# Kernel tuning notes

Measured on AMD Instinct MI355X. Metric: run time of the kernel, lower is better.

## Reference

```python
import jax, jax.numpy as jnp
import numpy as np

N = 100000   # nodes
E = 1600000  # edges
F_IN = 4
H = 64
G = 1000     # graphs in batch
C = 3        # num_classes
L = 2        # num_unit (LEConv layers)


def setup_inputs() -> dict:
    key = jax.random.key(0)
    ks = jax.random.split(key, 14)
    s = 0.1
    return {
        "x": jax.random.normal(ks[0], (N, F_IN), jnp.float32),
        "edge_index": jax.random.randint(ks[1], (2, E), 0, N, dtype=jnp.int32),
        "edge_attr": jax.random.uniform(ks[2], (E,), jnp.float32),
        "batch": jnp.sort(jax.random.randint(ks[3], (N,), 0, G, dtype=jnp.int32)),
        "w_emb": jax.random.normal(ks[4], (F_IN, H), jnp.float32) * s,
        "b_emb": jnp.zeros((H,), jnp.float32),
        "lin1_w": jax.random.normal(ks[5], (L, H, H), jnp.float32) * s,
        "lin1_b": jnp.zeros((L, H), jnp.float32),
        "lin2_w": jax.random.normal(ks[6], (L, H, H), jnp.float32) * s,  # bias=False in PyG LEConv
        "lin3_w": jax.random.normal(ks[7], (L, H, H), jnp.float32) * s,
        "lin3_b": jnp.zeros((L, H), jnp.float32),
        "mlp_w1": jax.random.normal(ks[8], (H, 2 * H), jnp.float32) * s,
        "mlp_b1": jnp.zeros((2 * H,), jnp.float32),
        "mlp_w2": jax.random.normal(ks[9], (2 * H, C), jnp.float32) * s,
        "mlp_b2": jnp.zeros((C,), jnp.float32),
    }


def reference(x, edge_index, edge_attr, batch, w_emb, b_emb,
              lin1_w, lin1_b, lin2_w, lin3_w, lin3_b,
              mlp_w1, mlp_b1, mlp_w2, mlp_b2):
    src, dst = edge_index[0], edge_index[1]  # message flows src(j) -> dst(i)
    h = x @ w_emb + b_emb  # [N, H]
    for l in range(L):
        a = h @ lin1_w[l] + lin1_b[l]            # lin1(x_j) source side
        b = h @ lin2_w[l]                         # lin2(x_i) target side, no bias
        msg = (a[src] - b[dst]) * edge_attr[:, None]   # [E, H]
        agg = jax.ops.segment_sum(msg, dst, num_segments=N)
        h = jax.nn.relu(agg + h @ lin3_w[l] + lin3_b[l])
    # global_mean_pool
    sums = jax.ops.segment_sum(h, batch, num_segments=G)        # [G, H]
    counts = jax.ops.segment_sum(jnp.ones((N,), h.dtype), batch, num_segments=G)
    graph_x = sums / jnp.maximum(counts, 1.0)[:, None]
    # causal_mlp head
    return jax.nn.relu(graph_x @ mlp_w1 + mlp_b1) @ mlp_w2 + mlp_b2  # [G, C]
```

## Files before the change

### kernel.cpp

```cpp
#include <hip/hip_runtime.h>

#define N_NODES 100000
#define N_EDGES 1600000
#define F_INPUT 4
#define HDIM 64
#define G_GRAPHS 1000
#define C_CLS 3

#define NPB 256
#define BSHIFT 8
#define NB 391
#define CBLK 98
#define CSR_CAP 6144
#define EMB_BLOCKS 6250
#define HIST_BLOCKS 512
#define BNDS_BLOCKS 391

typedef __attribute__((ext_vector_type(8))) short bf16x8;
typedef __attribute__((ext_vector_type(4))) float f32x4;

__device__ __forceinline__ unsigned short f2bf(float f) {
    unsigned u = __float_as_uint(f);
    unsigned r = (u + 0x7FFF + ((u >> 16) & 1)) >> 16;
    return (unsigned short)r;
}
__device__ __forceinline__ float bflo(unsigned u) {
    return __uint_as_float(u << 16);
}
__device__ __forceinline__ float bfhi(unsigned u) {
    return __uint_as_float(u & 0xFFFF0000u);
}
__device__ __forceinline__ float bf1(unsigned short s) {
    return __uint_as_float(((unsigned)s) << 16);
}

__global__ __launch_bounds__(256) void k_emb_hist(
    const float* __restrict__ x, const float* __restrict__ w, const float* __restrict__ b,
    unsigned short* __restrict__ h, const int* __restrict__ dst, int* __restrict__ bcnt,
    const int* __restrict__ batch, int* __restrict__ goff) {
    __shared__ int s[NB];
    if (blockIdx.x < EMB_BLOCKS) {
        int t = blockIdx.x * 256 + threadIdx.x;
        int n = t >> 4, f0 = (t & 15) * 4;
        const float* xr = x + n * F_INPUT;
        float x0 = xr[0], x1 = xr[1], x2 = xr[2], x3 = xr[3];
        ushort4 o;
        {
            float a0 = b[f0+0] + x0*w[0*HDIM+f0+0] + x1*w[1*HDIM+f0+0] + x2*w[2*HDIM+f0+0] + x3*w[3*HDIM+f0+0];
            float a1 = b[f0+1] + x0*w[0*HDIM+f0+1] + x1*w[1*HDIM+f0+1] + x2*w[2*HDIM+f0+1] + x3*w[3*HDIM+f0+1];
            float a2 = b[f0+2] + x0*w[0*HDIM+f0+2] + x1*w[1*HDIM+f0+2] + x2*w[2*HDIM+f0+2] + x3*w[3*HDIM+f0+2];
            float a3 = b[f0+3] + x0*w[0*HDIM+f0+3] + x1*w[1*HDIM+f0+3] + x2*w[2*HDIM+f0+3] + x3*w[3*HDIM+f0+3];
            o.x = f2bf(a0); o.y = f2bf(a1); o.z = f2bf(a2); o.w = f2bf(a3);
        }
        *(ushort4*)(h + (size_t)n * HDIM + f0) = o;
    } else if (blockIdx.x < EMB_BLOCKS + HIST_BLOCKS) {
        int bb = blockIdx.x - EMB_BLOCKS;
        for (int i = threadIdx.x; i < NB; i += 256) s[i] = 0;
        __syncthreads();
        for (int e = bb * 256 + threadIdx.x; e < N_EDGES; e += HIST_BLOCKS * 256)
            atomicAdd(&s[dst[e] >> BSHIFT], 1);
        __syncthreads();
        for (int i = threadIdx.x; i < NB; i += 256)
            if (s[i]) atomicAdd(&bcnt[i], s[i]);
    } else {
        int n = (blockIdx.x - EMB_BLOCKS - HIST_BLOCKS) * 256 + threadIdx.x;
        if (n >= N_NODES) return;
        int bv = batch[n];
        int bp = (n == 0) ? -1 : batch[n - 1];
        for (int g = bp + 1; g <= bv; ++g) goff[g] = n;
        if (n == N_NODES - 1) {
            for (int g = bv + 1; g <= G_GRAPHS; ++g) goff[g] = N_NODES;
        }
    }
}

__global__ __launch_bounds__(512) void k_boff(
    const int* __restrict__ bcnt, int* __restrict__ boff, int* __restrict__ bcur) {
    __shared__ int s[512];
    int t = threadIdx.x;
    int v = (t < NB) ? bcnt[t] : 0;
    s[t] = v;
    __syncthreads();
    for (int d = 1; d < 512; d <<= 1) {
        int x2 = (t >= d) ? s[t - d] : 0;
        __syncthreads();
        s[t] += x2;
        __syncthreads();
    }
    int ex = s[t] - v;
    if (t < NB) { boff[t] = ex; bcur[t] = ex; }
    if (t == 0) boff[NB] = N_EDGES;
}

__global__ __launch_bounds__(1024) void k_bucket(const int* __restrict__ src,
                                                 const int* __restrict__ dst,
                                                 const float* __restrict__ attr,
                                                 int* __restrict__ bcur,
                                                 int2* __restrict__ bbuf) {
    __shared__ int cnt[NB];
    __shared__ int base[NB];
    for (int i = threadIdx.x; i < NB; i += 1024) cnt[i] = 0;
    __syncthreads();
    int e0 = blockIdx.x * 16384;
    int myb[16], myrank[16];
    int2 mypack[16];
#pragma unroll
    for (int k = 0; k < 16; ++k) {
        int e = e0 + k * 1024 + threadIdx.x;
        if (e < N_EDGES) {
            int d = dst[e];
            int b = d >> BSHIFT;
            myb[k] = b;
            myrank[k] = atomicAdd(&cnt[b], 1);
            mypack[k].x = src[e] | ((d & (NPB - 1)) << 17);
            mypack[k].y = __float_as_int(attr[e]);
        } else
            myb[k] = -1;
    }
    __syncthreads();
    for (int i = threadIdx.x; i < NB; i += 1024)
        base[i] = cnt[i] ? atomicAdd(&bcur[i], cnt[i]) : 0;
    __syncthreads();
#pragma unroll
    for (int k = 0; k < 16; ++k)
        if (myb[k] >= 0) bbuf[base[myb[k]] + myrank[k]] = mypack[k];
}

__global__ __launch_bounds__(256) void k_csr(const int2* __restrict__ bbuf,
                                             const int* __restrict__ boff,
                                             int* __restrict__ off,
                                             float* __restrict__ wsum,
                                             int2* __restrict__ edge2) {
    __shared__ int2 se[CSR_CAP];
    __shared__ int deg[NPB];
    __shared__ float wsm[NPB];
    __shared__ int loff[NPB];
    __shared__ int sct[256];
    int b = blockIdx.x;
    int lo = boff[b];
    int cnt = boff[b + 1] - lo;
    if (cnt > CSR_CAP) cnt = CSR_CAP;
    int t = threadIdx.x;
    deg[t] = 0;
    wsm[t] = 0.f;
    for (int i = t; i < cnt; i += 256) se[i] = bbuf[lo + i];
    __syncthreads();
    for (int i = t; i < cnt; i += 256) {
        int2 p = se[i];
        int dloc = (p.x >> 17) & (NPB - 1);
        atomicAdd(&deg[dloc], 1);
        atomicAdd(&wsm[dloc], __int_as_float(p.y));
    }
    __syncthreads();
    int v = deg[t];
    sct[t] = v;
    __syncthreads();
    for (int d = 1; d < 256; d <<= 1) {
        int x2 = (t >= d) ? sct[t - d] : 0;
        __syncthreads();
        sct[t] += x2;
        __syncthreads();
    }
    int ex = sct[t] - v;
    loff[t] = ex;
    __syncthreads();
    int n = b * NPB + t;
    if (n < N_NODES) { off[n] = lo + ex; wsum[n] = wsm[t]; }
    if (b == NB - 1 && t == 0) off[N_NODES] = N_EDGES;
    deg[t] = 0;
    __syncthreads();
    for (int i = t; i < cnt; i += 256) {
        int2 p = se[i];
        int dloc = (p.x >> 17) & (NPB - 1);
        int r = atomicAdd(&deg[dloc], 1);
        edge2[lo + loff[dloc] + r] = make_int2(p.x & 0x1FFFF, p.y);
    }
}

__global__ __launch_bounds__(256) void k_gemm3(
    const unsigned short* __restrict__ h,
    const float* __restrict__ W1, const float* __restrict__ b1,
    const float* __restrict__ W2,
    const float* __restrict__ W3, const float* __restrict__ b3,
    const float* __restrict__ wsum,
    unsigned short* __restrict__ a_out, unsigned short* __restrict__ d_out_) {
    int wave = threadIdx.x >> 6;
    int lane = threadIdx.x & 63;
    int row = lane & 15;
    int kg = lane >> 4;
    int base = blockIdx.x * 64;
    int col = wave * 16 + row;

    bf16x8 Bf[3][2];
    const float* Ws[3] = {W1, W2, W3};
#pragma unroll
    for (int m = 0; m < 3; ++m)
#pragma unroll
        for (int hf = 0; hf < 2; ++hf) {
            union { bf16x8 v; unsigned short u[8]; } fr;
#pragma unroll
            for (int j = 0; j < 8; ++j) {
                int k = hf * 32 + kg * 8 + j;
                fr.u[j] = f2bf(Ws[m][k * HDIM + col]);
            }
            Bf[m][hf] = fr.v;
        }

    float bias1 = b1[col];
    float bias3 = b3[col];

    f32x4 acc[3][4];
#pragma unroll
    for (int m = 0; m < 3; ++m)
#pragma unroll
        for (int t = 0; t < 4; ++t) acc[m][t] = (f32x4){0.f, 0.f, 0.f, 0.f};

#pragma unroll
    for (int t = 0; t < 4; ++t) {
        int n = base + t * 16 + row;
        bf16x8 a0, a1;
        if (n < N_NODES) {
            const unsigned short* hr = h + (size_t)n * HDIM;
            a0 = *(const bf16x8*)(hr + kg * 8);
            a1 = *(const bf16x8*)(hr + 32 + kg * 8);
        } else {
            a0 = (bf16x8){0,0,0,0,0,0,0,0};
            a1 = (bf16x8){0,0,0,0,0,0,0,0};
        }
#pragma unroll
        for (int m = 0; m < 3; ++m) {
            acc[m][t] = __builtin_amdgcn_mfma_f32_16x16x32_bf16(a0, Bf[m][0], acc[m][t], 0, 0, 0);
            acc[m][t] = __builtin_amdgcn_mfma_f32_16x16x32_bf16(a1, Bf[m][1], acc[m][t], 0, 0, 0);
        }
    }

#pragma unroll
    for (int t = 0; t < 4; ++t) {
#pragma unroll
        for (int r = 0; r < 4; ++r) {
            int n = base + t * 16 + kg * 4 + r;
            if (n >= N_NODES) continue;
            float ws = wsum[n];
            float av = acc[0][t][r] + bias1;
            float dv = acc[2][t][r] + bias3 - acc[1][t][r] * ws;
            a_out[(size_t)n * HDIM + col] = f2bf(av);
            d_out_[(size_t)n * HDIM + col] = f2bf(dv);
        }
    }
}

__global__ __launch_bounds__(256) void k_agg(const int2* __restrict__ edge2,
                                             const int* __restrict__ off,
                                             const unsigned short* __restrict__ a,
                                             const unsigned short* __restrict__ dbuf,
                                             unsigned short* __restrict__ h) {
    int wid = threadIdx.x >> 6;
    int lane = threadIdx.x & 63;
    int slot = lane >> 3;
    int fo = lane & 7;
    int n = blockIdx.x * 4 + wid;
    if (n >= N_NODES) return;
    int lo = off[n], hi = off[n + 1];

    float acc[8];
#pragma unroll
    for (int q = 0; q < 8; ++q) acc[q] = 0.f;

#define GATHER_ADD(J)                                                        \
    if ((J) < hi) {                                                          \
        int2 p = edge2[(J)];                                                 \
        float w = __int_as_float(p.y);                                       \
        uint4 u = *(const uint4*)(a + (size_t)p.x * HDIM + fo * 8);          \
        acc[0] += bflo(u.x) * w; acc[1] += bfhi(u.x) * w;                    \
        acc[2] += bflo(u.y) * w; acc[3] += bfhi(u.y) * w;                    \
        acc[4] += bflo(u.z) * w; acc[5] += bfhi(u.z) * w;                    \
        acc[6] += bflo(u.w) * w; acc[7] += bfhi(u.w) * w;                    \
    }

    for (int j0 = lo; j0 < hi; j0 += 32) {
        GATHER_ADD(j0 + slot)
        GATHER_ADD(j0 + 8 + slot)
        GATHER_ADD(j0 + 16 + slot)
        GATHER_ADD(j0 + 24 + slot)
    }
#undef GATHER_ADD

#pragma unroll
    for (int m = 8; m <= 32; m <<= 1) {
#pragma unroll
        for (int q = 0; q < 8; ++q) acc[q] += __shfl_xor(acc[q], m);
    }

    if (slot == 0) {
        size_t o = (size_t)n * HDIM + fo * 8;
        uint4 dv = *(const uint4*)(dbuf + o);
        float dd[8] = {bflo(dv.x), bfhi(dv.x), bflo(dv.y), bfhi(dv.y),
                       bflo(dv.z), bfhi(dv.z), bflo(dv.w), bfhi(dv.w)};
        unsigned r[4];
#pragma unroll
        for (int q = 0; q < 4; ++q) {
            unsigned lo16 = f2bf(fmaxf(acc[2 * q] + dd[2 * q], 0.f));
            unsigned hi16 = f2bf(fmaxf(acc[2 * q + 1] + dd[2 * q + 1], 0.f));
            r[q] = lo16 | (hi16 << 16);
        }
        *(uint4*)(h + o) = make_uint4(r[0], r[1], r[2], r[3]);
    }
}

__global__ __launch_bounds__(256) void k_poolhead(const unsigned short* __restrict__ h,
                                                  const int* __restrict__ goff,
                                                  const float* __restrict__ W1,
                                                  const float* __restrict__ b1,
                                                  const float* __restrict__ W2,
                                                  const float* __restrict__ b2,
                                                  float* __restrict__ out) {
    int g = blockIdx.x;
    __shared__ float part[256];
    __shared__ float sx[HDIM];
    __shared__ float sy[2 * HDIM];
    int t = threadIdx.x;
    int lo = goff[g], hi = goff[g + 1];
    int f = t & 63, quarter = t >> 6;
    float acc = 0.f;
    for (int n = lo + quarter; n < hi; n += 4) acc += bf1(h[(size_t)n * HDIM + f]);
    part[t] = acc;
    __syncthreads();
    if (t < HDIM)
        sx[t] = (part[t] + part[t + 64] + part[t + 128] + part[t + 192]) /
                fmaxf((float)(hi - lo), 1.f);
    __syncthreads();
    if (t < 2 * HDIM) {
        float a1 = b1[t];
        for (int k = 0; k < HDIM; ++k) a1 += sx[k] * W1[k * 2 * HDIM + t];
        sy[t] = fmaxf(a1, 0.f);
    }
    __syncthreads();
    if (t < C_CLS) {
        float o = b2[t];
        for (int k = 0; k < 2 * HDIM; ++k) o += sy[k] * W2[k * C_CLS + t];
        out[g * C_CLS + t] = o;
    }
}

extern "C" void kernel_launch(void* const* d_in, const int* in_sizes, int n_in,
                              void* d_out, int out_size, void* d_ws, size_t ws_size,
                              hipStream_t stream) {
    const float* x      = (const float*)d_in[0];
    const int*   ei     = (const int*)d_in[1];
    const float* eattr  = (const float*)d_in[2];
    const int*   batch  = (const int*)d_in[3];
    const float* w_emb  = (const float*)d_in[4];
    const float* b_emb  = (const float*)d_in[5];
    const float* lin1_w = (const float*)d_in[6];
    const float* lin1_b = (const float*)d_in[7];
    const float* lin2_w = (const float*)d_in[8];
    const float* lin3_w = (const float*)d_in[9];
    const float* lin3_b = (const float*)d_in[10];
    const float* mlp_w1 = (const float*)d_in[11];
    const float* mlp_b1 = (const float*)d_in[12];
    const float* mlp_w2 = (const float*)d_in[13];
    const float* mlp_b2 = (const float*)d_in[14];
    float* out = (float*)d_out;

    const int* src = ei;
    const int* dst = ei + N_EDGES;

    const size_t NH = (size_t)N_NODES * HDIM;
    unsigned short* h   = (unsigned short*)d_ws;
    unsigned short* dbf = h + NH;
    unsigned short* abf = dbf + NH;
    float* wsum = (float*)(abf + NH);
    int2* edge2 = (int2*)(wsum + N_NODES);
    int2* bbuf  = edge2 + N_EDGES;
    int* off    = (int*)(bbuf + N_EDGES);
    int* bcnt   = off + N_NODES + 1;
    int* bcur   = bcnt + NB;
    int* boff   = bcur + NB;
    int* goff   = boff + NB + 1;

    hipMemsetAsync(bcnt, 0, NB * sizeof(int), stream);

    k_emb_hist<<<EMB_BLOCKS + HIST_BLOCKS + BNDS_BLOCKS, 256, 0, stream>>>(
        x, w_emb, b_emb, h, dst, bcnt, batch, goff);
    k_boff<<<1, 512, 0, stream>>>(bcnt, boff, bcur);
    k_bucket<<<CBLK, 1024, 0, stream>>>(src, dst, eattr, bcur, bbuf);
    k_csr<<<NB, 256, 0, stream>>>(bbuf, boff, off, wsum, edge2);

    int gemm_blocks = (N_NODES + 63) / 64;
    int agg_blocks = (N_NODES + 3) / 4;

    for (int l = 0; l < 2; ++l) {
        const float* W1 = lin1_w + l * HDIM * HDIM;
        const float* B1 = lin1_b + l * HDIM;
        const float* W2 = lin2_w + l * HDIM * HDIM;
        const float* W3 = lin3_w + l * HDIM * HDIM;
        const float* B3 = lin3_b + l * HDIM;
        k_gemm3<<<gemm_blocks, 256, 0, stream>>>(h, W1, B1, W2, W3, B3, wsum, abf, dbf);
        k_agg<<<agg_blocks, 256, 0, stream>>>(edge2, off, abf, dbf, h);
    }

    k_poolhead<<<G_GRAPHS, 256, 0, stream>>>(h, goff, mlp_w1, mlp_b1, mlp_w2, mlp_b2, out);
}
```

Measured before the change: 235.3 us.

## Fold embedding into first-layer weights and fuse aggregation with next-layer GEMM

A tiny kernel pre-multiplies the embedding weights and bias into the three layer-0 linear maps. The first GEMM can then run directly on the 4-feature input, and the embedding pass that wrote h to memory is removed. The layer-0 aggregation is fused with the layer-1 three-way GEMM: each block aggregates 16 nodes into shared memory and immediately runs MFMA on them, so h is never written to or re-read from global memory. The risks are lower occupancy and serialized per-wave node loops in the fused kernel, and the fused grid assumes N is divisible by 16.

```diff
diff --git a/kernel.cpp b/kernel.cpp
--- a/kernel.cpp
+++ b/kernel.cpp
@@ -12,7 +12,6 @@
 #define NB 391
 #define CBLK 98
 #define CSR_CAP 6144
-#define EMB_BLOCKS 6250
 #define HIST_BLOCKS 512
 #define BNDS_BLOCKS 391
 
@@ -34,27 +33,39 @@
     return __uint_as_float(((unsigned)s) << 16);
 }
 
-__global__ __launch_bounds__(256) void k_emb_hist(
-    const float* __restrict__ x, const float* __restrict__ w, const float* __restrict__ b,
-    unsigned short* __restrict__ h, const int* __restrict__ dst, int* __restrict__ bcnt,
+__global__ __launch_bounds__(256) void k_prew(
+    const float* __restrict__ w_emb, const float* __restrict__ b_emb,
+    const float* __restrict__ lin1_w, const float* __restrict__ lin1_b,
+    const float* __restrict__ lin2_w,
+    const float* __restrict__ lin3_w, const float* __restrict__ lin3_b,
+    float* __restrict__ wp, float* __restrict__ bp) {
+    int t = threadIdx.x;
+    int k = t >> 6, f = t & 63;
+    const float* Ws[3] = {lin1_w, lin2_w, lin3_w};
+#pragma unroll
+    for (int m = 0; m < 3; ++m) {
+        float s = 0.f;
+        for (int j = 0; j < HDIM; ++j) s += w_emb[k * HDIM + j] * Ws[m][j * HDIM + f];
+        wp[m * 256 + k * HDIM + f] = s;
+    }
+    if (t < HDIM) {
+#pragma unroll
+        for (int m = 0; m < 3; ++m) {
+            float s = 0.f;
+            for (int j = 0; j < HDIM; ++j) s += b_emb[j] * Ws[m][j * HDIM + t];
+            if (m == 0) s += lin1_b[t];
+            if (m == 2) s += lin3_b[t];
+            bp[m * HDIM + t] = s;
+        }
+    }
+}
+
+__global__ __launch_bounds__(256) void k_hist_bounds(
+    const int* __restrict__ dst, int* __restrict__ bcnt,
     const int* __restrict__ batch, int* __restrict__ goff) {
     __shared__ int s[NB];
-    if (blockIdx.x < EMB_BLOCKS) {
-        int t = blockIdx.x * 256 + threadIdx.x;
-        int n = t >> 4, f0 = (t & 15) * 4;
-        const float* xr = x + n * F_INPUT;
-        float x0 = xr[0], x1 = xr[1], x2 = xr[2], x3 = xr[3];
-        ushort4 o;
-        {
-            float a0 = b[f0+0] + x0*w[0*HDIM+f0+0] + x1*w[1*HDIM+f0+0] + x2*w[2*HDIM+f0+0] + x3*w[3*HDIM+f0+0];
-            float a1 = b[f0+1] + x0*w[0*HDIM+f0+1] + x1*w[1*HDIM+f0+1] + x2*w[2*HDIM+f0+1] + x3*w[3*HDIM+f0+1];
-            float a2 = b[f0+2] + x0*w[0*HDIM+f0+2] + x1*w[1*HDIM+f0+2] + x2*w[2*HDIM+f0+2] + x3*w[3*HDIM+f0+2];
-            float a3 = b[f0+3] + x0*w[0*HDIM+f0+3] + x1*w[1*HDIM+f0+3] + x2*w[2*HDIM+f0+3] + x3*w[3*HDIM+f0+3];
-            o.x = f2bf(a0); o.y = f2bf(a1); o.z = f2bf(a2); o.w = f2bf(a3);
-        }
-        *(ushort4*)(h + (size_t)n * HDIM + f0) = o;
-    } else if (blockIdx.x < EMB_BLOCKS + HIST_BLOCKS) {
-        int bb = blockIdx.x - EMB_BLOCKS;
+    if (blockIdx.x < HIST_BLOCKS) {
+        int bb = blockIdx.x;
         for (int i = threadIdx.x; i < NB; i += 256) s[i] = 0;
         __syncthreads();
         for (int e = bb * 256 + threadIdx.x; e < N_EDGES; e += HIST_BLOCKS * 256)
@@ -63,11 +74,11 @@
         for (int i = threadIdx.x; i < NB; i += 256)
             if (s[i]) atomicAdd(&bcnt[i], s[i]);
     } else {
-        int n = (blockIdx.x - EMB_BLOCKS - HIST_BLOCKS) * 256 + threadIdx.x;
+        int n = (blockIdx.x - HIST_BLOCKS) * 256 + threadIdx.x;
         if (n >= N_NODES) return;
         int bv = batch[n];
-        int bp = (n == 0) ? -1 : batch[n - 1];
-        for (int g = bp + 1; g <= bv; ++g) goff[g] = n;
+        int bp_ = (n == 0) ? -1 : batch[n - 1];
+        for (int g = bp_ + 1; g <= bv; ++g) goff[g] = n;
         if (n == N_NODES - 1) {
             for (int g = bv + 1; g <= G_GRAPHS; ++g) goff[g] = N_NODES;
         }
@@ -177,12 +188,9 @@
     }
 }
 
-__global__ __launch_bounds__(256) void k_gemm3(
-    const unsigned short* __restrict__ h,
-    const float* __restrict__ W1, const float* __restrict__ b1,
-    const float* __restrict__ W2,
-    const float* __restrict__ W3, const float* __restrict__ b3,
-    const float* __restrict__ wsum,
+__global__ __launch_bounds__(256) void k_gemm1st(
+    const float* __restrict__ x, const float* __restrict__ wp,
+    const float* __restrict__ bp, const float* __restrict__ wsum,
     unsigned short* __restrict__ a_out, unsigned short* __restrict__ d_out_) {
     int wave = threadIdx.x >> 6;
     int lane = threadIdx.x & 63;
@@ -191,6 +199,119 @@
     int base = blockIdx.x * 64;
     int col = wave * 16 + row;
 
+    bf16x8 Bf[3];
+#pragma unroll
+    for (int m = 0; m < 3; ++m) {
+        union { bf16x8 v; unsigned short u[8]; } fr;
+#pragma unroll
+        for (int j = 0; j < 8; ++j)
+            fr.u[j] = (kg == 0 && j < F_INPUT) ? f2bf(wp[m * 256 + j * HDIM + col]) : 0;
+        Bf[m] = fr.v;
+    }
+    float bias1 = bp[col], bias2 = bp[HDIM + col], bias3 = bp[2 * HDIM + col];
+
+    f32x4 acc[3][4];
+#pragma unroll
+    for (int m = 0; m < 3; ++m)
+#pragma unroll
+        for (int t = 0; t < 4; ++t) acc[m][t] = (f32x4){0.f, 0.f, 0.f, 0.f};
+
+#pragma unroll
+    for (int t = 0; t < 4; ++t) {
+        int n = base + t * 16 + row;
+        union { bf16x8 v; unsigned short u[8]; } af;
+#pragma unroll
+        for (int j = 0; j < 8; ++j) af.u[j] = 0;
+        if (kg == 0 && n < N_NODES) {
+            float4 xv = *(const float4*)(x + (size_t)n * F_INPUT);
+            af.u[0] = f2bf(xv.x); af.u[1] = f2bf(xv.y);
+            af.u[2] = f2bf(xv.z); af.u[3] = f2bf(xv.w);
+        }
+#pragma unroll
+        for (int m = 0; m < 3; ++m)
+            acc[m][t] = __builtin_amdgcn_mfma_f32_16x16x32_bf16(af.v, Bf[m], acc[m][t], 0, 0, 0);
+    }
+
+#pragma unroll
+    for (int t = 0; t < 4; ++t) {
+#pragma unroll
+        for (int r = 0; r < 4; ++r) {
+            int n = base + t * 16 + kg * 4 + r;
+            if (n >= N_NODES) continue;
+            float ws = wsum[n];
+            float av = acc[0][t][r] + bias1;
+            float dv = acc[2][t][r] + bias3 - (acc[1][t][r] + bias2) * ws;
+            a_out[(size_t)n * HDIM + col] = f2bf(av);
+            d_out_[(size_t)n * HDIM + col] = f2bf(dv);
+        }
+    }
+}
+
+__global__ __launch_bounds__(256) void k_aggemm(
+    const int2* __restrict__ edge2, const int* __restrict__ off,
+    const unsigned short* __restrict__ a, const unsigned short* __restrict__ dbuf,
+    const float* __restrict__ W1, const float* __restrict__ b1,
+    const float* __restrict__ W2,
+    const float* __restrict__ W3, const float* __restrict__ b3,
+    const float* __restrict__ wsum,
+    unsigned short* __restrict__ a_out, unsigned short* __restrict__ d_out_) {
+    __shared__ unsigned short ht[16 * 72];
+    int tid = threadIdx.x;
+    int wid = tid >> 6, lane = tid & 63;
+    int slot = lane >> 3, fo = lane & 7;
+    int base = blockIdx.x * 16;
+
+    for (int nn = 0; nn < 4; ++nn) {
+        int n = base + wid * 4 + nn;
+        int lo = off[n], hi = off[n + 1];
+        float acc[8];
+#pragma unroll
+        for (int q = 0; q < 8; ++q) acc[q] = 0.f;
+
+#define GATHER_ADD(J)                                                        \
+    if ((J) < hi) {                                                          \
+        int2 p = edge2[(J)];                                                 \
+        float w = __int_as_float(p.y);                                       \
+        uint4 u = *(const uint4*)(a + (size_t)p.x * HDIM + fo * 8);          \
+        acc[0] += bflo(u.x) * w; acc[1] += bfhi(u.x) * w;                    \
+        acc[2] += bflo(u.y) * w; acc[3] += bfhi(u.y) * w;                    \
+        acc[4] += bflo(u.z) * w; acc[5] += bfhi(u.z) * w;                    \
+        acc[6] += bflo(u.w) * w; acc[7] += bfhi(u.w) * w;                    \
+    }
+        for (int j0 = lo; j0 < hi; j0 += 32) {
+            GATHER_ADD(j0 + slot)
+            GATHER_ADD(j0 + 8 + slot)
+            GATHER_ADD(j0 + 16 + slot)
+            GATHER_ADD(j0 + 24 + slot)
+        }
+#undef GATHER_ADD
+
+#pragma unroll
+        for (int m = 8; m <= 32; m <<= 1) {
+#pragma unroll
+            for (int q = 0; q < 8; ++q) acc[q] += __shfl_xor(acc[q], m);
+        }
+
+        if (slot == 0) {
+            size_t o = (size_t)n * HDIM + fo * 8;
+            uint4 dv = *(const uint4*)(dbuf + o);
+            float dd[8] = {bflo(dv.x), bfhi(dv.x), bflo(dv.y), bfhi(dv.y),
+                           bflo(dv.z), bfhi(dv.z), bflo(dv.w), bfhi(dv.w)};
+            unsigned r[4];
+#pragma unroll
+            for (int q = 0; q < 4; ++q) {
+                unsigned lo16 = f2bf(fmaxf(acc[2 * q] + dd[2 * q], 0.f));
+                unsigned hi16 = f2bf(fmaxf(acc[2 * q + 1] + dd[2 * q + 1], 0.f));
+                r[q] = lo16 | (hi16 << 16);
+            }
+            *(uint4*)(&ht[(wid * 4 + nn) * 72 + fo * 8]) = make_uint4(r[0], r[1], r[2], r[3]);
+        }
+    }
+    __syncthreads();
+
+    int row = lane & 15, kg = lane >> 4;
+    int col = wid * 16 + row;
+
     bf16x8 Bf[3][2];
     const float* Ws[3] = {W1, W2, W3};
 #pragma unroll
@@ -206,46 +327,27 @@
             Bf[m][hf] = fr.v;
         }
 
+    bf16x8 a0 = *(const bf16x8*)(&ht[row * 72 + kg * 8]);
+    bf16x8 a1 = *(const bf16x8*)(&ht[row * 72 + 32 + kg * 8]);
+
+    f32x4 acc3[3];
+#pragma unroll
+    for (int m = 0; m < 3; ++m) {
+        acc3[m] = (f32x4){0.f, 0.f, 0.f, 0.f};
+        acc3[m] = __builtin_amdgcn_mfma_f32_16x16x32_bf16(a0, Bf[m][0], acc3[m], 0, 0, 0);
+        acc3[m] = __builtin_amdgcn_mfma_f32_16x16x32_bf16(a1, Bf[m][1], acc3[m], 0, 0, 0);
+    }
+
     float bias1 = b1[col];
     float bias3 = b3[col];
-
-    f32x4 acc[3][4];
-#pragma unroll
-    for (int m = 0; m < 3; ++m)
-#pragma unroll
-        for (int t = 0; t < 4; ++t) acc[m][t] = (f32x4){0.f, 0.f, 0.f, 0.f};
-
-#pragma unroll
-    for (int t = 0; t < 4; ++t) {
-        int n = base + t * 16 + row;
-        bf16x8 a0, a1;
-        if (n < N_NODES) {
-            const unsigned short* hr = h + (size_t)n * HDIM;
-            a0 = *(const bf16x8*)(hr + kg * 8);
-            a1 = *(const bf16x8*)(hr + 32 + kg * 8);
-        } else {
-            a0 = (bf16x8){0,0,0,0,0,0,0,0};
-            a1 = (bf16x8){0,0,0,0,0,0,0,0};
-        }
-#pragma unroll
-        for (int m = 0; m < 3; ++m) {
-            acc[m][t] = __builtin_amdgcn_mfma_f32_16x16x32_bf16(a0, Bf[m][0], acc[m][t], 0, 0, 0);
-            acc[m][t] = __builtin_amdgcn_mfma_f32_16x16x32_bf16(a1, Bf[m][1], acc[m][t], 0, 0, 0);
-        }
-    }
-
-#pragma unroll
-    for (int t = 0; t < 4; ++t) {
-#pragma unroll
-        for (int r = 0; r < 4; ++r) {
-            int n = base + t * 16 + kg * 4 + r;
-            if (n >= N_NODES) continue;
-            float ws = wsum[n];
-            float av = acc[0][t][r] + bias1;
-            float dv = acc[2][t][r] + bias3 - acc[1][t][r] * ws;
-            a_out[(size_t)n * HDIM + col] = f2bf(av);
-            d_out_[(size_t)n * HDIM + col] = f2bf(dv);
-        }
+#pragma unroll
+    for (int r = 0; r < 4; ++r) {
+        int n = base + kg * 4 + r;
+        float ws = wsum[n];
+        float av = acc3[0][r] + bias1;
+        float dv = acc3[2][r] + bias3 - acc3[1][r] * ws;
+        a_out[(size_t)n * HDIM + col] = f2bf(av);
+        d_out_[(size_t)n * HDIM + col] = f2bf(dv);
     }
 }
 
@@ -276,7 +378,6 @@
         acc[4] += bflo(u.z) * w; acc[5] += bfhi(u.z) * w;                    \
         acc[6] += bflo(u.w) * w; acc[7] += bfhi(u.w) * w;                    \
     }
-
     for (int j0 = lo; j0 < hi; j0 += 32) {
         GATHER_ADD(j0 + slot)
         GATHER_ADD(j0 + 8 + slot)
@@ -366,10 +467,12 @@
     const int* dst = ei + N_EDGES;
 
     const size_t NH = (size_t)N_NODES * HDIM;
-    unsigned short* h   = (unsigned short*)d_ws;
-    unsigned short* dbf = h + NH;
-    unsigned short* abf = dbf + NH;
-    float* wsum = (float*)(abf + NH);
+    unsigned short* abf0 = (unsigned short*)d_ws;
+    unsigned short* dbf0 = abf0 + NH;
+    unsigned short* abf1 = dbf0 + NH;
+    unsigned short* dbf1 = abf1 + NH;
+    unsigned short* h2   = dbf1 + NH;
+    float* wsum = (float*)(h2 + NH);
     int2* edge2 = (int2*)(wsum + N_NODES);
     int2* bbuf  = edge2 + N_EDGES;
     int* off    = (int*)(bbuf + N_EDGES);
@@ -377,27 +480,28 @@
     int* bcur   = bcnt + NB;
     int* boff   = bcur + NB;
     int* goff   = boff + NB + 1;
+    float* wp   = (float*)(goff + G_GRAPHS + 1);
+    float* bp   = wp + 3 * 256;
 
     hipMemsetAsync(bcnt, 0, NB * sizeof(int), stream);
 
-    k_emb_hist<<<EMB_BLOCKS + HIST_BLOCKS + BNDS_BLOCKS, 256, 0, stream>>>(
-        x, w_emb, b_emb, h, dst, bcnt, batch, goff);
+    k_prew<<<1, 256, 0, stream>>>(w_emb, b_emb,
+                                  lin1_w, lin1_b, lin2_w, lin3_w, lin3_b, wp, bp);
+    k_hist_bounds<<<HIST_BLOCKS + BNDS_BLOCKS, 256, 0, stream>>>(dst, bcnt, batch, goff);
     k_boff<<<1, 512, 0, stream>>>(bcnt, boff, bcur);
     k_bucket<<<CBLK, 1024, 0, stream>>>(src, dst, eattr, bcur, bbuf);
     k_csr<<<NB, 256, 0, stream>>>(bbuf, boff, off, wsum, edge2);
 
     int gemm_blocks = (N_NODES + 63) / 64;
+    int aggemm_blocks = N_NODES / 16;
     int agg_blocks = (N_NODES + 3) / 4;
 
-    for (int l = 0; l < 2; ++l) {
-        const float* W1 = lin1_w + l * HDIM * HDIM;
-        const float* B1 = lin1_b + l * HDIM;
-        const float* W2 = lin2_w + l * HDIM * HDIM;
-        const float* W3 = lin3_w + l * HDIM * HDIM;
-        const float* B3 = lin3_b + l * HDIM;
-        k_gemm3<<<gemm_blocks, 256, 0, stream>>>(h, W1, B1, W2, W3, B3, wsum, abf, dbf);
-        k_agg<<<agg_blocks, 256, 0, stream>>>(edge2, off, abf, dbf, h);
-    }
-
-    k_poolhead<<<G_GRAPHS, 256, 0, stream>>>(h, goff, mlp_w1, mlp_b1, mlp_w2, mlp_b2, out);
-}
+    k_gemm1st<<<gemm_blocks, 256, 0, stream>>>(x, wp, bp, wsum, abf0, dbf0);
+    k_aggemm<<<aggemm_blocks, 256, 0, stream>>>(edge2, off, abf0, dbf0,
+                                                lin1_w + HDIM * HDIM, lin1_b + HDIM,
+                                                lin2_w + HDIM * HDIM,
+                                                lin3_w + HDIM * HDIM, lin3_b + HDIM,
+                                                wsum, abf1, dbf1);
+    k_agg<<<agg_blocks, 256, 0, stream>>>(edge2, off, abf1, dbf1, h2);
+    k_poolhead<<<G_GRAPHS, 256, 0, stream>>>(h2, goff, mlp_w1, mlp_b1, mlp_w2, mlp_b2, out);
+}
```

Result: no change. 231.3 us (-1.7%).

## Fold embedding into first-layer weights and fuse layer-0 GEMM into CSR kernel

Applied to the files above, without the earlier changes.

Precomputes w_emb@lin{1,2,3}_w and the matching biases in a tiny kernel, so layer 0's a/d projections come straight from the 4-dim input x via a K=4 MFMA. That work runs at the tail of the CSR-build kernel, which already holds wsum in shared memory. This drops the embedding pass, the write and read of h, and one full 64x64 GEMM launch. The memset is also folded into the prew kernel. The trade-offs are extra bf16 rounding of x and of the folded weights, and the CSR blocks now do the 256-node MFMA epilogue serially.

```diff
diff --git a/kernel.cpp b/kernel.cpp
--- a/kernel.cpp
+++ b/kernel.cpp
@@ -12,7 +12,6 @@
 #define NB 391
 #define CBLK 98
 #define CSR_CAP 6144
-#define EMB_BLOCKS 6250
 #define HIST_BLOCKS 512
 #define BNDS_BLOCKS 391
 
@@ -34,27 +33,40 @@
     return __uint_as_float(((unsigned)s) << 16);
 }
 
-__global__ __launch_bounds__(256) void k_emb_hist(
-    const float* __restrict__ x, const float* __restrict__ w, const float* __restrict__ b,
-    unsigned short* __restrict__ h, const int* __restrict__ dst, int* __restrict__ bcnt,
+__global__ __launch_bounds__(256) void k_prew(
+    const float* __restrict__ w_emb, const float* __restrict__ b_emb,
+    const float* __restrict__ lin1_w, const float* __restrict__ lin1_b,
+    const float* __restrict__ lin2_w,
+    const float* __restrict__ lin3_w, const float* __restrict__ lin3_b,
+    float* __restrict__ wp, float* __restrict__ bp, int* __restrict__ bcnt) {
+    int t = threadIdx.x;
+    for (int i = t; i < NB; i += 256) bcnt[i] = 0;
+    int k = t >> 6, f = t & 63;
+    const float* Ws[3] = {lin1_w, lin2_w, lin3_w};
+#pragma unroll
+    for (int m = 0; m < 3; ++m) {
+        float s = 0.f;
+        for (int j = 0; j < HDIM; ++j) s += w_emb[k * HDIM + j] * Ws[m][j * HDIM + f];
+        wp[m * 256 + k * HDIM + f] = s;
+    }
+    if (t < HDIM) {
+#pragma unroll
+        for (int m = 0; m < 3; ++m) {
+            float s = 0.f;
+            for (int j = 0; j < HDIM; ++j) s += b_emb[j] * Ws[m][j * HDIM + t];
+            if (m == 0) s += lin1_b[t];
+            if (m == 2) s += lin3_b[t];
+            bp[m * HDIM + t] = s;
+        }
+    }
+}
+
+__global__ __launch_bounds__(256) void k_hist_bounds(
+    const int* __restrict__ dst, int* __restrict__ bcnt,
     const int* __restrict__ batch, int* __restrict__ goff) {
     __shared__ int s[NB];
-    if (blockIdx.x < EMB_BLOCKS) {
-        int t = blockIdx.x * 256 + threadIdx.x;
-        int n = t >> 4, f0 = (t & 15) * 4;
-        const float* xr = x + n * F_INPUT;
-        float x0 = xr[0], x1 = xr[1], x2 = xr[2], x3 = xr[3];
-        ushort4 o;
-        {
-            float a0 = b[f0+0] + x0*w[0*HDIM+f0+0] + x1*w[1*HDIM+f0+0] + x2*w[2*HDIM+f0+0] + x3*w[3*HDIM+f0+0];
-            float a1 = b[f0+1] + x0*w[0*HDIM+f0+1] + x1*w[1*HDIM+f0+1] + x2*w[2*HDIM+f0+1] + x3*w[3*HDIM+f0+1];
-            float a2 = b[f0+2] + x0*w[0*HDIM+f0+2] + x1*w[1*HDIM+f0+2] + x2*w[2*HDIM+f0+2] + x3*w[3*HDIM+f0+2];
-            float a3 = b[f0+3] + x0*w[0*HDIM+f0+3] + x1*w[1*HDIM+f0+3] + x2*w[2*HDIM+f0+3] + x3*w[3*HDIM+f0+3];
-            o.x = f2bf(a0); o.y = f2bf(a1); o.z = f2bf(a2); o.w = f2bf(a3);
-        }
-        *(ushort4*)(h + (size_t)n * HDIM + f0) = o;
-    } else if (blockIdx.x < EMB_BLOCKS + HIST_BLOCKS) {
-        int bb = blockIdx.x - EMB_BLOCKS;
+    if (blockIdx.x < HIST_BLOCKS) {
+        int bb = blockIdx.x;
         for (int i = threadIdx.x; i < NB; i += 256) s[i] = 0;
         __syncthreads();
         for (int e = bb * 256 + threadIdx.x; e < N_EDGES; e += HIST_BLOCKS * 256)
@@ -63,11 +75,11 @@
         for (int i = threadIdx.x; i < NB; i += 256)
             if (s[i]) atomicAdd(&bcnt[i], s[i]);
     } else {
-        int n = (blockIdx.x - EMB_BLOCKS - HIST_BLOCKS) * 256 + threadIdx.x;
+        int n = (blockIdx.x - HIST_BLOCKS) * 256 + threadIdx.x;
         if (n >= N_NODES) return;
         int bv = batch[n];
-        int bp = (n == 0) ? -1 : batch[n - 1];
-        for (int g = bp + 1; g <= bv; ++g) goff[g] = n;
+        int bp_ = (n == 0) ? -1 : batch[n - 1];
+        for (int g = bp_ + 1; g <= bv; ++g) goff[g] = n;
         if (n == N_NODES - 1) {
             for (int g = bv + 1; g <= G_GRAPHS; ++g) goff[g] = N_NODES;
         }
@@ -130,7 +142,12 @@
                                              const int* __restrict__ boff,
                                              int* __restrict__ off,
                                              float* __restrict__ wsum,
-                                             int2* __restrict__ edge2) {
+                                             int2* __restrict__ edge2,
+                                             const float* __restrict__ x,
+                                             const float* __restrict__ wp,
+                                             const float* __restrict__ bp,
+                                             unsigned short* __restrict__ a_out,
+                                             unsigned short* __restrict__ d_out_) {
     __shared__ int2 se[CSR_CAP];
     __shared__ int deg[NPB];
     __shared__ float wsm[NPB];
@@ -164,8 +181,8 @@
     int ex = sct[t] - v;
     loff[t] = ex;
     __syncthreads();
-    int n = b * NPB + t;
-    if (n < N_NODES) { off[n] = lo + ex; wsum[n] = wsm[t]; }
+    int n0 = b * NPB + t;
+    if (n0 < N_NODES) { off[n0] = lo + ex; wsum[n0] = wsm[t]; }
     if (b == NB - 1 && t == 0) off[N_NODES] = N_EDGES;
     deg[t] = 0;
     __syncthreads();
@@ -174,6 +191,51 @@
         int dloc = (p.x >> 17) & (NPB - 1);
         int r = atomicAdd(&deg[dloc], 1);
         edge2[lo + loff[dloc] + r] = make_int2(p.x & 0x1FFFF, p.y);
+    }
+
+    {
+        int wave = t >> 6, lane = t & 63;
+        int row = lane & 15, kg = lane >> 4;
+        int col = wave * 16 + row;
+        bf16x8 Bf[3];
+#pragma unroll
+        for (int m = 0; m < 3; ++m) {
+            union { bf16x8 v; unsigned short u[8]; } fr;
+#pragma unroll
+            for (int j = 0; j < 8; ++j)
+                fr.u[j] = (kg == 0 && j < F_INPUT) ? f2bf(wp[m * 256 + j * HDIM + col])
+                                                   : (unsigned short)0;
+            Bf[m] = fr.v;
+        }
+        float bias1 = bp[col], bias2 = bp[HDIM + col], bias3 = bp[2 * HDIM + col];
+        int base = b * NPB;
+        for (int tt = 0; tt < 16; ++tt) {
+            int n = base + tt * 16 + row;
+            union { bf16x8 v; unsigned short u[8]; } af;
+#pragma unroll
+            for (int j = 0; j < 8; ++j) af.u[j] = 0;
+            if (kg == 0 && n < N_NODES) {
+                float4 xv = *(const float4*)(x + (size_t)n * F_INPUT);
+                af.u[0] = f2bf(xv.x); af.u[1] = f2bf(xv.y);
+                af.u[2] = f2bf(xv.z); af.u[3] = f2bf(xv.w);
+            }
+            f32x4 ac0 = (f32x4){0.f, 0.f, 0.f, 0.f};
+            f32x4 ac1 = (f32x4){0.f, 0.f, 0.f, 0.f};
+            f32x4 ac2 = (f32x4){0.f, 0.f, 0.f, 0.f};
+            ac0 = __builtin_amdgcn_mfma_f32_16x16x32_bf16(af.v, Bf[0], ac0, 0, 0, 0);
+            ac1 = __builtin_amdgcn_mfma_f32_16x16x32_bf16(af.v, Bf[1], ac1, 0, 0, 0);
+            ac2 = __builtin_amdgcn_mfma_f32_16x16x32_bf16(af.v, Bf[2], ac2, 0, 0, 0);
+#pragma unroll
+            for (int r = 0; r < 4; ++r) {
+                int nn = base + tt * 16 + kg * 4 + r;
+                if (nn >= N_NODES) continue;
+                float ws = wsm[tt * 16 + kg * 4 + r];
+                float av = ac0[r] + bias1;
+                float dv = ac2[r] + bias3 - (ac1[r] + bias2) * ws;
+                a_out[(size_t)nn * HDIM + col] = f2bf(av);
+                d_out_[(size_t)nn * HDIM + col] = f2bf(dv);
+            }
+        }
     }
 }
 
@@ -366,10 +428,10 @@
     const int* dst = ei + N_EDGES;
 
     const size_t NH = (size_t)N_NODES * HDIM;
-    unsigned short* h   = (unsigned short*)d_ws;
-    unsigned short* dbf = h + NH;
-    unsigned short* abf = dbf + NH;
-    float* wsum = (float*)(abf + NH);
+    unsigned short* abf = (unsigned short*)d_ws;
+    unsigned short* dbf = abf + NH;
+    unsigned short* h   = dbf + NH;
+    float* wsum = (float*)(h + NH);
     int2* edge2 = (int2*)(wsum + N_NODES);
     int2* bbuf  = edge2 + N_EDGES;
     int* off    = (int*)(bbuf + N_EDGES);
@@ -377,27 +439,24 @@
     int* bcur   = bcnt + NB;
     int* boff   = bcur + NB;
     int* goff   = boff + NB + 1;
-
-    hipMemsetAsync(bcnt, 0, NB * sizeof(int), stream);
-
-    k_emb_hist<<<EMB_BLOCKS + HIST_BLOCKS + BNDS_BLOCKS, 256, 0, stream>>>(
-        x, w_emb, b_emb, h, dst, bcnt, batch, goff);
+    float* wp   = (float*)(goff + G_GRAPHS + 1);
+    float* bp   = wp + 3 * 256;
+
+    k_prew<<<1, 256, 0, stream>>>(w_emb, b_emb,
+                                  lin1_w, lin1_b, lin2_w, lin3_w, lin3_b, wp, bp, bcnt);
+    k_hist_bounds<<<HIST_BLOCKS + BNDS_BLOCKS, 256, 0, stream>>>(dst, bcnt, batch, goff);
     k_boff<<<1, 512, 0, stream>>>(bcnt, boff, bcur);
     k_bucket<<<CBLK, 1024, 0, stream>>>(src, dst, eattr, bcur, bbuf);
-    k_csr<<<NB, 256, 0, stream>>>(bbuf, boff, off, wsum, edge2);
+    k_csr<<<NB, 256, 0, stream>>>(bbuf, boff, off, wsum, edge2, x, wp, bp, abf, dbf);
 
     int gemm_blocks = (N_NODES + 63) / 64;
     int agg_blocks = (N_NODES + 3) / 4;
 
-    for (int l = 0; l < 2; ++l) {
-        const float* W1 = lin1_w + l * HDIM * HDIM;
-        const float* B1 = lin1_b + l * HDIM;
-        const float* W2 = lin2_w + l * HDIM * HDIM;
-        const float* W3 = lin3_w + l * HDIM * HDIM;
-        const float* B3 = lin3_b + l * HDIM;
-        k_gemm3<<<gemm_blocks, 256, 0, stream>>>(h, W1, B1, W2, W3, B3, wsum, abf, dbf);
-        k_agg<<<agg_blocks, 256, 0, stream>>>(edge2, off, abf, dbf, h);
-    }
-
+    k_agg<<<agg_blocks, 256, 0, stream>>>(edge2, off, abf, dbf, h);
+    k_gemm3<<<gemm_blocks, 256, 0, stream>>>(h, lin1_w + HDIM * HDIM, lin1_b + HDIM,
+                                             lin2_w + HDIM * HDIM,
+                                             lin3_w + HDIM * HDIM, lin3_b + HDIM,
+                                             wsum, abf, dbf);
+    k_agg<<<agg_blocks, 256, 0, stream>>>(edge2, off, abf, dbf, h);
     k_poolhead<<<G_GRAPHS, 256, 0, stream>>>(h, goff, mlp_w1, mlp_b1, mlp_w2, mlp_b2, out);
 }
```

New measurement: 234.9 us. About the same (-0.2%).
